# Kernel tuning notes

Measured on AMD Instinct MI355X. Metric: run time of the kernel, lower is better.

Reference implementation:

```python
import jax, jax.numpy as jnp
import numpy as np

N_ATOMS = 16384
B_GRAPHS = 64
K_CLUSTERS = 64          # clusters per molecule
M_CLUSTERS = B_GRAPHS * K_CLUSTERS
HID = 256                # hidden_channels (== node_attr feature dim)
FIL = 256                # num_filters
ECH = 64                 # edge_channels (num gaussians)
L_INT = 6                # num_interactions
CUTOFF = 10.0
LN2 = float(np.log(2.0))


def _ssp(x):
    # ShiftedSoftplus
    return jax.nn.softplus(x) - LN2


def setup_inputs() -> dict:
    key = jax.random.key(0)
    ks = jax.random.split(key, 12)
    pos = jax.random.normal(ks[0], (N_ATOMS, 3), jnp.float32) * 2.0
    node_attr = jax.random.normal(ks[1], (N_ATOMS, HID), jnp.float32)
    atoms_per_cluster = N_ATOMS // M_CLUSTERS
    subgraph_index = (jnp.arange(N_ATOMS) // atoms_per_cluster).astype(jnp.int64)
    batch = (jnp.arange(N_ATOMS) // (N_ATOMS // B_GRAPHS)).astype(jnp.int64)
    s = 0.05
    params = {
        "mlp_w1": jax.random.normal(ks[2], (L_INT, ECH, FIL), jnp.float32) * s,
        "mlp_b1": jnp.zeros((L_INT, FIL), jnp.float32),
        "mlp_w2": jax.random.normal(ks[3], (L_INT, FIL, FIL), jnp.float32) * s,
        "mlp_b2": jnp.zeros((L_INT, FIL), jnp.float32),
        "lin1_w": jax.random.normal(ks[4], (L_INT, HID, FIL), jnp.float32) * s,  # no bias
        "lin2_w": jax.random.normal(ks[5], (L_INT, FIL, HID), jnp.float32) * s,
        "lin2_b": jnp.zeros((L_INT, HID), jnp.float32),
        "lin_w":  jax.random.normal(ks[6], (L_INT, HID, HID), jnp.float32) * s,
        "lin_b":  jnp.zeros((L_INT, HID), jnp.float32),
    }
    return {"pos": pos, "node_attr": node_attr,
            "subgraph_index": subgraph_index, "batch": batch,
            "num_graphs": B_GRAPHS, "clusters_per_graph": K_CLUSTERS, **params}


def _complete_graph_edges(num_graphs, clusters_per_graph):
    # static (numpy) construction of per-molecule complete graph, no self loops
    K = clusters_per_graph
    i = np.arange(K)
    pr, pc = np.meshgrid(i, i, indexing='ij')
    m = pr != pc
    pr, pc = pr[m], pc[m]                       # (K*(K-1),)
    off = np.arange(num_graphs)[:, None] * K    # (B,1)
    row = jnp.asarray((off + pr[None, :]).reshape(-1))
    col = jnp.asarray((off + pc[None, :]).reshape(-1))
    return row, col


def reference(pos, node_attr, subgraph_index, batch, num_graphs, clusters_per_graph,
              mlp_w1, mlp_b1, mlp_w2, mlp_b2, lin1_w, lin2_w, lin2_b, lin_w, lin_b):
    M = num_graphs * clusters_per_graph
    # ---- coarse_grain: scatter-mean atoms into clusters ----
    cnt = jax.ops.segment_sum(jnp.ones((pos.shape[0],), pos.dtype), subgraph_index, num_segments=M)
    cnt = jnp.maximum(cnt, 1.0)[:, None]
    cluster_pos = jax.ops.segment_sum(pos, subgraph_index, num_segments=M) / cnt        # (M,3)
    cluster_attr = jax.ops.segment_sum(node_attr, subgraph_index, num_segments=M) / cnt  # (M,H)

    # ---- complete graph per molecule ----
    row, col = _complete_graph_edges(num_graphs, clusters_per_graph)
    edge_length = jnp.linalg.norm(cluster_pos[row] - cluster_pos[col], axis=1)          # (E,)

    # ---- GaussianSmearing ----
    offset = jnp.linspace(0.0, CUTOFF, ECH)
    coeff = -0.5 / (offset[1] - offset[0]) ** 2
    edge_attr = jnp.exp(coeff * (edge_length[:, None] - offset[None, :]) ** 2)          # (E,ECH)

    # smooth cutoff envelope
    C = 0.5 * (jnp.cos(edge_length * jnp.pi / CUTOFF) + 1.0)
    C = C * (edge_length <= CUTOFF).astype(C.dtype)                                     # (E,)

    # ---- SchNetEncoder (embed_node=False) ----
    h = cluster_attr
    for l in range(L_INT):
        # filter-generating MLP
        W = _ssp(edge_attr @ mlp_w1[l] + mlp_b1[l]) @ mlp_w2[l] + mlp_b2[l]             # (E,F)
        W = W * C[:, None]
        x = h @ lin1_w[l]                                                               # (M,F)
        agg = jax.ops.segment_sum(x[row] * W, col, num_segments=M)                      # (M,F)
        x = agg @ lin2_w[l] + lin2_b[l]                                                 # (M,H)
        x = _ssp(x)
        x = x @ lin_w[l] + lin_b[l]
        h = h + x                                                                       # residual
    return h
```

## Files before the change

kernel.cpp:

```cpp
#include <hip/hip_runtime.h>
#include <cstdint>

#define NATOMS 16384
#define BGRAPH 64
#define KC     64
#define MCL    (BGRAPH*KC)
#define HIDC   256
#define FILC   256
#define ECHC   64
#define LINT   6

#define TGRID  1024
#define TROWS  1088
#define NBP    1056

typedef __bf16 bf16x8 __attribute__((ext_vector_type(8)));
typedef __bf16 bf16x2 __attribute__((ext_vector_type(2)));
typedef float  f32x4  __attribute__((ext_vector_type(4)));
typedef unsigned short u16x8 __attribute__((ext_vector_type(8)));

__device__ __forceinline__ float bf2f(unsigned short u) {
    unsigned int x = ((unsigned int)u) << 16;
    return __builtin_bit_cast(float, x);
}
__device__ __forceinline__ unsigned short f2bf(float f) {
    __bf16 h = (__bf16)f;
    return __builtin_bit_cast(unsigned short, h);
}
__device__ __forceinline__ unsigned int pk2(float a, float b) {
    bf16x2 v = { (__bf16)a, (__bf16)b };
    return __builtin_bit_cast(unsigned int, v);
}
__device__ __forceinline__ float ssp_poly(float x) {
    float u = fminf(x * x, 4.0f);
    float q = u * fmaf(u, fmaf(u, 3.4722222e-4f, -5.2083333e-3f), 0.125f);
    return fmaf(0.5f, x, q);
}
__device__ __forceinline__ float ssp_fast(float x) {
    float m = fmaxf(x, 0.0f);
    float t = __builtin_amdgcn_exp2f(-fabsf(x) * 1.44269504088896341f);
    float l = __builtin_amdgcn_logf(1.0f + t);
    return fmaf(0.69314718055994531f, l, m - 0.69314718055994531f);
}
__device__ __forceinline__ int sw_off(int row, int col) {
    int s = (row + (row >> 3)) & 7;
    return row * 256 + ((((col >> 3) ^ s) << 3) | (col & 7));
}
__device__ __forceinline__ int phi_sw(int row) {
    return ((row & 7) ^ ((row >> 3) & 7)) & 7;
}

#define CGB   1024
#define N_W1  (LINT*16384)
#define N_BIG (LINT*65536)
#define PACK_BLOCKS ((N_W1 + 4*N_BIG + 255)/256)
__global__ void k_prep(const float* __restrict__ pos, const float* __restrict__ attr,
                       const int* __restrict__ subi,
                       float* __restrict__ h, unsigned short* __restrict__ h_bf,
                       float* __restrict__ cpos,
                       const float* __restrict__ w1_src, const float* __restrict__ w2_src,
                       const float* __restrict__ l1_src, const float* __restrict__ l2_src,
                       const float* __restrict__ lw_src,
                       unsigned short* __restrict__ w1p, unsigned short* __restrict__ w2p,
                       unsigned short* __restrict__ l1p, unsigned short* __restrict__ l2p,
                       unsigned short* __restrict__ lwp)
{
    if (blockIdx.x >= CGB) {
        int idx = (blockIdx.x - CGB) * 256 + threadIdx.x;
        if (idx < N_W1) {
            int j = idx & 7, lane = (idx >> 3) & 63, kt = (idx >> 9) & 1;
            int mt = (idx >> 10) & 15, l = idx >> 14;
            int ech = kt*32 + (lane >> 4)*8 + j;
            int f1  = mt*16 + (lane & 15);
            w1p[idx] = f2bf(w1_src[(l*64 + ech)*256 + f1]);
            return;
        }
        int r = idx - N_W1;
        int which = r / N_BIG;
        if (which >= 4) return;
        int e = r - which * N_BIG;
        const float* src = (which == 0) ? w2_src : (which == 1) ? l1_src
                         : (which == 2) ? l2_src : lw_src;
        unsigned short* dst = (which == 0) ? w2p : (which == 1) ? l1p
                            : (which == 2) ? l2p : lwp;
        int n = e % 256;
        int k = (e / 256) % 256;
        int l = e / 65536;
        int nt = n >> 4, kt = k >> 5, q = (k >> 3) & 3, j = k & 7;
        int lane = q*16 + (n & 15);
        dst[l*65536 + ((nt*8 + kt)*64 + lane)*8 + j] = f2bf(src[e]);
        return;
    }
    const int m = blockIdx.x * 4 + (threadIdx.x >> 6);
    const int lane = threadIdx.x & 63;
    const bool is64 = (subi[8] == 1);
    int lo = 0, hi = NATOMS;
    while (lo < hi) { int mid = (lo + hi) >> 1;
        int v = is64 ? subi[2*mid] : subi[mid];
        if (v < m) lo = mid + 1; else hi = mid; }
    int lo2 = lo, hi2 = NATOMS;
    while (lo2 < hi2) { int mid = (lo2 + hi2) >> 1;
        int v = is64 ? subi[2*mid] : subi[mid];
        if (v < m + 1) lo2 = mid + 1; else hi2 = mid; }
    const int cnt2 = lo2 - lo;
    const float inv = 1.0f / (float)(cnt2 > 0 ? cnt2 : 1);

    float4 s = {0.f, 0.f, 0.f, 0.f};
    for (int a = lo; a < lo2; a++) {
        const float4 v = *reinterpret_cast<const float4*>(&attr[a*HIDC + lane*4]);
        s.x += v.x; s.y += v.y; s.z += v.z; s.w += v.w;
    }
    s.x *= inv; s.y *= inv; s.z *= inv; s.w *= inv;
    *reinterpret_cast<float4*>(&h[m*HIDC + lane*4]) = s;
    const int o = m*HIDC + lane*4;
    h_bf[o+0] = f2bf(s.x); h_bf[o+1] = f2bf(s.y);
    h_bf[o+2] = f2bf(s.z); h_bf[o+3] = f2bf(s.w);
    if (lane < 3) {
        float p = 0.f;
        for (int a = lo; a < lo2; a++) p += pos[a*3 + lane];
        cpos[m*3 + lane] = p * inv;
    }
}

#define OSTR 264
__global__ __launch_bounds__(512, 6) void k_tab(
    const unsigned short* __restrict__ w1p_all, const unsigned short* __restrict__ w2p_all,
    const float* __restrict__ b1_all, const float* __restrict__ b2_all,
    unsigned short* __restrict__ table)
{
    __shared__ unsigned short G_s[64 * 256];
    __shared__ unsigned short phi_s[16 * OSTR];
    __shared__ float C_s[64];
    __shared__ float d_s[64];

    const int l  = blockIdx.x / 17;
    const int g0 = (blockIdx.x % 17) * 64;
    const unsigned short* w1p = w1p_all + (size_t)l*16384;
    const unsigned short* w2p = w2p_all + (size_t)l*65536;
    const float* b1 = b1_all + l*256;
    const float* b2 = b2_all + l*256;

    const int t  = threadIdx.x;
    const int w  = t >> 6, lane = t & 63;
    const int quad = lane >> 4, l16 = lane & 15;

    if (t < 64) {
        float d = (float)(g0 + t) * 0.009765625f;
        d_s[t] = d;
        float Cv = 0.5f * (__cosf(d * 0.31415926535897932f) + 1.0f);
        C_s[t] = (d <= 10.0f) ? Cv : 0.0f;
    }
    __syncthreads();

    const float DELTA = 10.0f / 63.0f;
    const float C2 = (-0.5f / (DELTA * DELTA)) * 1.44269504088896341f;
    {
        float d = d_s[lane];
        u16x8 ph;
        #pragma unroll
        for (int j = 0; j < 8; j++) {
            float diff = d - (float)(w*8 + j) * DELTA;
            ph[j] = f2bf(__builtin_amdgcn_exp2f(C2 * diff * diff));
        }
        *reinterpret_cast<u16x8*>(&phi_s[lane*64 + ((w ^ phi_sw(lane)) << 3)]) = ph;
    }
    __syncthreads();

    f32x4 acc1[2][4];
    #pragma unroll
    for (int mt = 0; mt < 2; mt++) {
        const int f1b = (w*2 + mt)*16 + quad*4;
        float4 bq = *reinterpret_cast<const float4*>(&b1[f1b]);
        #pragma unroll
        for (int nt = 0; nt < 4; nt++) {
            acc1[mt][nt][0] = bq.x; acc1[mt][nt][1] = bq.y;
            acc1[mt][nt][2] = bq.z; acc1[mt][nt][3] = bq.w;
        }
    }
    #pragma unroll
    for (int kt = 0; kt < 2; kt++) {
        bf16x8 bfr[4];
        #pragma unroll
        for (int nt = 0; nt < 4; nt++) {
            int row = nt*16 + l16;
            bfr[nt] = *reinterpret_cast<const bf16x8*>(
                &phi_s[row*64 + (((kt*4 + quad) ^ phi_sw(row)) << 3)]);
        }
        #pragma unroll
        for (int mt = 0; mt < 2; mt++) {
            bf16x8 afr = *reinterpret_cast<const bf16x8*>(
                w1p + (((w*2 + mt)*2 + kt)*64 + lane)*8);
            #pragma unroll
            for (int nt = 0; nt < 4; nt++)
                acc1[mt][nt] = __builtin_amdgcn_mfma_f32_16x16x32_bf16(afr, bfr[nt], acc1[mt][nt], 0, 0, 0);
        }
    }

    float Cn[4];
    #pragma unroll
    for (int nt = 0; nt < 4; nt++) Cn[nt] = C_s[nt*16 + l16];

    #pragma unroll
    for (int mt = 0; mt < 2; mt++) {
        const int f1b = (w*2 + mt)*16 + quad*4;
        #pragma unroll
        for (int nt = 0; nt < 4; nt++) {
            float v0 = ssp_poly(acc1[mt][nt][0]) * Cn[nt];
            float v1 = ssp_poly(acc1[mt][nt][1]) * Cn[nt];
            float v2 = ssp_poly(acc1[mt][nt][2]) * Cn[nt];
            float v3 = ssp_poly(acc1[mt][nt][3]) * Cn[nt];
            uint2 pp;
            pp.x = pk2(v0, v1);
            pp.y = pk2(v2, v3);
            int edge = nt*16 + l16;
            int s = (edge + (edge >> 3)) & 7;
            int a = edge*256 + ((((f1b >> 3) ^ s) << 3) | (f1b & 7));
            *reinterpret_cast<uint2*>(&G_s[a]) = pp;
        }
    }
    __syncthreads();

    f32x4 acc2[4][2];
    #pragma unroll
    for (int a = 0; a < 4; a++)
        #pragma unroll
        for (int bb = 0; bb < 2; bb++) acc2[a][bb] = f32x4{0.f,0.f,0.f,0.f};

    #pragma unroll
    for (int kt = 0; kt < 8; kt++) {
        bf16x8 afr[4];
        #pragma unroll
        for (int mt = 0; mt < 4; mt++) {
            int row = mt*16 + l16;
            int s = (row + (row >> 3)) & 7;
            afr[mt] = *reinterpret_cast<const bf16x8*>(&G_s[row*256 + (((kt*4 + quad) ^ s) << 3)]);
        }
        #pragma unroll
        for (int nt = 0; nt < 2; nt++) {
            const int ntg = w*2 + nt;
            bf16x8 bfr = *reinterpret_cast<const bf16x8*>(w2p + ((ntg*8 + kt)*64 + lane)*8);
            #pragma unroll
            for (int mt = 0; mt < 4; mt++)
                acc2[mt][nt] = __builtin_amdgcn_mfma_f32_16x16x32_bf16(afr[mt], bfr, acc2[mt][nt], 0, 0, 0);
        }
    }

    #pragma unroll
    for (int nt = 0; nt < 2; nt++) {
        const int f = (w*2 + nt)*16 + l16;
        const float b2v = b2[f];
        #pragma unroll
        for (int mt = 0; mt < 4; mt++) {
            #pragma unroll
            for (int i = 0; i < 4; i++) {
                int e = mt*16 + quad*4 + i;
                table[((size_t)l*TROWS + g0 + e)*256 + f] =
                    f2bf(fmaf(C_s[e], b2v, acc2[mt][nt][i]));
            }
        }
    }
}

__device__ __forceinline__ void gemm16(const unsigned short* A_s, const unsigned short* Bp,
                                       int w, int lane, f32x4 acc[4])
{
    const int quad = lane >> 4, l16 = lane & 15;
    const int s = (l16 + (l16 >> 3)) & 7;
    #pragma unroll
    for (int nt = 0; nt < 4; nt++) acc[nt] = f32x4{0.f,0.f,0.f,0.f};
    #pragma unroll
    for (int kt = 0; kt < 8; kt++) {
        bf16x8 afr = *reinterpret_cast<const bf16x8*>(&A_s[l16*256 + (((kt*4 + quad) ^ s) << 3)]);
        #pragma unroll
        for (int nt = 0; nt < 4; nt++) {
            bf16x8 bfr = *reinterpret_cast<const bf16x8*>(Bp + (((w*4 + nt)*8 + kt)*64 + lane)*8);
            acc[nt] = __builtin_amdgcn_mfma_f32_16x16x32_bf16(afr, bfr, acc[nt], 0, 0, 0);
        }
    }
}
__device__ __forceinline__ void gemm16w16(const unsigned short* A_s, const unsigned short* Bp,
                                          int w, int lane, f32x4& acc)
{
    const int quad = lane >> 4, l16 = lane & 15;
    const int s = (l16 + (l16 >> 3)) & 7;
    acc = f32x4{0.f,0.f,0.f,0.f};
    #pragma unroll
    for (int kt = 0; kt < 8; kt++) {
        bf16x8 afr = *reinterpret_cast<const bf16x8*>(&A_s[l16*256 + (((kt*4 + quad) ^ s) << 3)]);
        bf16x8 bfr = *reinterpret_cast<const bf16x8*>(Bp + (((w*8 + kt)*64 + lane))*8);
        acc = __builtin_amdgcn_mfma_f32_16x16x32_bf16(afr, bfr, acc, 0, 0, 0);
    }
}

#define PK_TOTAL (LINT*NBP*32)
#define PK_BLOCKS ((PK_TOTAL + 255)/256)
__global__ __launch_bounds__(256) void k_gemm0p(
    const unsigned short* __restrict__ A_bf, const unsigned short* __restrict__ Bp,
    unsigned short* __restrict__ out_bf,
    const unsigned short* __restrict__ table, unsigned short* __restrict__ tbl2)
{
    if (blockIdx.x >= 256) {
        int idx = (blockIdx.x - 256) * 256 + threadIdx.x;
        if (idx >= PK_TOTAL) return;
        int fc = idx & 31;
        int qq = idx >> 5;
        int bin = qq % NBP;
        int l = qq / NBP;
        if (bin > TGRID) return;
        const unsigned short* Ts = table + ((size_t)l*TROWS + bin)*256 + fc*8;
        u16x8 a = *reinterpret_cast<const u16x8*>(Ts);
        u16x8 b = *reinterpret_cast<const u16x8*>(Ts + 256);
        u16x8 d;
        #pragma unroll
        for (int j = 0; j < 8; j++) d[j] = f2bf(bf2f(b[j]) - bf2f(a[j]));
        unsigned short* dst = tbl2 + ((size_t)l*NBP + bin)*512 + fc*16;
        *reinterpret_cast<u16x8*>(dst)     = a;
        *reinterpret_cast<u16x8*>(dst + 8) = d;
        return;
    }
    __shared__ unsigned short A_s[16 * 256];
    const int mb = blockIdx.x;
    const int t = threadIdx.x;
    const int w = t >> 6, lane = t & 63, quad = lane >> 4, l16 = lane & 15;

    {
        int r = t >> 4, seg = t & 15;
        int s = (r + (r >> 3)) & 7;
        const u16x8* src = reinterpret_cast<const u16x8*>(A_bf + (size_t)(mb*16 + r)*256 + seg*16);
        int c = seg*2;
        *reinterpret_cast<u16x8*>(&A_s[r*256 + (((c  ) ^ s) << 3)]) = src[0];
        *reinterpret_cast<u16x8*>(&A_s[r*256 + (((c+1) ^ s) << 3)]) = src[1];
    }
    __syncthreads();

    f32x4 acc[4];
    gemm16(A_s, Bp, w, lane, acc);

    #pragma unroll
    for (int nt = 0; nt < 4; nt++)
        #pragma unroll
        for (int i = 0; i < 4; i++) {
            int rg = mb*16 + quad*4 + i;
            int col = w*64 + nt*16 + l16;
            out_bf[(size_t)rg*256 + col] = f2bf(acc[nt][i]);
        }
}

template<int DO_X>
__global__ __launch_bounds__(1024) void k_layer(
    const float* __restrict__ cpos,
    const unsigned short* __restrict__ xin, unsigned short* __restrict__ xout,
    const unsigned short* __restrict__ Tp,
    const unsigned short* __restrict__ lin2p, const float* __restrict__ lin2_b,
    const unsigned short* __restrict__ linp,  const float* __restrict__ lin_b,
    const unsigned short* __restrict__ lin1p,
    float* __restrict__ h)
{
    __shared__ unsigned short x_s[64 * 256];
    __shared__ unsigned short A0[16 * 256];
    __shared__ unsigned short A1[16 * 256];
    __shared__ int   idx_s[1024];
    __shared__ float frac_s[1024];

    const int blk = blockIdx.x;
    const int b = blk >> 2, q = blk & 3;
    const int t = threadIdx.x;
    const int w = t >> 6, lane = t & 63, quad = lane >> 4, l16 = lane & 15;

    {
        int r = t >> 4, seg = t & 15;
        const u16x8* s8 = reinterpret_cast<const u16x8*>(
            xin + ((size_t)(b*64 + r))*256 + seg*16);
        u16x8* dst = reinterpret_cast<u16x8*>(&x_s[r*256 + seg*16]);
        dst[0] = s8[0]; dst[1] = s8[1];
    }
    {
        int r = t >> 4, cc = t & 15;
        int gr = b*64 + r, gc = b*64 + q*16 + cc;
        float ax = cpos[gr*3 + 0] - cpos[gc*3 + 0];
        float ay = cpos[gr*3 + 1] - cpos[gc*3 + 1];
        float az = cpos[gr*3 + 2] - cpos[gc*3 + 2];
        float d = sqrtf(ax*ax + ay*ay + az*az);
        int i; float fr;
        if (gr == gc || d >= 10.0f) { i = TGRID; fr = 0.0f; }
        else {
            float u = d * 102.4f;
            i = (int)u; fr = u - (float)i;
        }
        idx_s[t] = i * 512; frac_s[t] = fr;
    }
    __syncthreads();

    const int fc  = t & 31;
    const int cp  = (t >> 5) & 7;
    const int dup = t >> 8;
    float s0[8] = {0.f,0.f,0.f,0.f,0.f,0.f,0.f,0.f};
    float s1[8] = {0.f,0.f,0.f,0.f,0.f,0.f,0.f,0.f};
    {
        const int rbase = dup * 16;
        const unsigned short* Tfc = Tp + fc*16;
        #pragma unroll 4
        for (int rr = 0; rr < 16; rr++) {
            const int r = rbase + rr;
            const int   p0 = idx_s [r*16 + cp];
            const float f0 = frac_s[r*16 + cp];
            const int   p1 = idx_s [r*16 + cp + 8];
            const float f1 = frac_s[r*16 + cp + 8];
            const u16x8 x8 = *reinterpret_cast<const u16x8*>(&x_s[r*256 + fc*8]);
            const u16x8 a0 = *reinterpret_cast<const u16x8*>(Tfc + p0);
            const u16x8 d0 = *reinterpret_cast<const u16x8*>(Tfc + p0 + 8);
            const u16x8 a1 = *reinterpret_cast<const u16x8*>(Tfc + p1);
            const u16x8 d1 = *reinterpret_cast<const u16x8*>(Tfc + p1 + 8);
            #pragma unroll
            for (int j = 0; j < 8; j++) {
                float xv = bf2f(x8[j]);
                float w0 = fmaf(f0, bf2f(d0[j]), bf2f(a0[j]));
                float w1 = fmaf(f1, bf2f(d1[j]), bf2f(a1[j]));
                s0[j] = fmaf(xv, w0, s0[j]);
                s1[j] = fmaf(xv, w1, s1[j]);
            }
        }
    }
    __syncthreads();
    {
        float* sc = reinterpret_cast<float*>(x_s);
        const int li = t & 255;
        if (dup & 1) {
            float* dst = sc + ((dup >> 1) << 12) + li*16;
            #pragma unroll
            for (int j = 0; j < 8; j++) { dst[j] = s0[j]; dst[8+j] = s1[j]; }
        }
        __syncthreads();
        if (!(dup & 1)) {
            const float* src = sc + ((dup >> 1) << 12) + li*16;
            #pragma unroll
            for (int j = 0; j < 8; j++) { s0[j] += src[j]; s1[j] += src[8+j]; }
        }
        __syncthreads();
        if (dup == 2) {
            float* dst = sc + li*16;
            #pragma unroll
            for (int j = 0; j < 8; j++) { dst[j] = s0[j]; dst[8+j] = s1[j]; }
        }
        __syncthreads();
        if (dup == 0) {
            const float* src = sc + li*16;
            u16x8 p0v, p1v;
            #pragma unroll
            for (int j = 0; j < 8; j++) {
                p0v[j] = f2bf(s0[j] + src[j]);
                p1v[j] = f2bf(s1[j] + src[8+j]);
            }
            const int c0 = cp, c1 = cp + 8;
            *reinterpret_cast<u16x8*>(&A0[c0*256 + ((fc ^ ((c0 + (c0>>3)) & 7)) << 3)]) = p0v;
            *reinterpret_cast<u16x8*>(&A0[c1*256 + ((fc ^ ((c1 + (c1>>3)) & 7)) << 3)]) = p1v;
        }
    }
    __syncthreads();

    const int col = w*16 + l16;
    const int rbase_g = b*64 + q*16;
    f32x4 acc;
    gemm16w16(A0, lin2p, w, lane, acc);
    float bv = lin2_b[col];
    #pragma unroll
    for (int i = 0; i < 4; i++)
        A1[sw_off(quad*4 + i, col)] = f2bf(ssp_fast(acc[i] + bv));
    __syncthreads();

    gemm16w16(A1, linp, w, lane, acc);
    bv = lin_b[col];
    float hv[4];
    #pragma unroll
    for (int i = 0; i < 4; i++) {
        int rg = rbase_g + quad*4 + i;
        float v = acc[i] + bv + h[(size_t)rg*256 + col];
        h[(size_t)rg*256 + col] = v;
        hv[i] = v;
    }
    if (DO_X) {
        #pragma unroll
        for (int i = 0; i < 4; i++)
            A0[sw_off(quad*4 + i, col)] = f2bf(hv[i]);
        __syncthreads();
        gemm16w16(A0, lin1p, w, lane, acc);
        #pragma unroll
        for (int i = 0; i < 4; i++) {
            int rg = rbase_g + quad*4 + i;
            xout[(size_t)rg*256 + col] = f2bf(acc[i]);
        }
    }
}

extern "C" void kernel_launch(void* const* d_in, const int* in_sizes, int n_in,
                              void* d_out, int out_size, void* d_ws, size_t ws_size,
                              hipStream_t stream)
{
    const float* pos    = (const float*)d_in[0];
    const float* nattr  = (const float*)d_in[1];
    const int*   subi   = (const int*)d_in[2];
    const float* mlp_w1 = (const float*)d_in[6];
    const float* mlp_b1 = (const float*)d_in[7];
    const float* mlp_w2 = (const float*)d_in[8];
    const float* mlp_b2 = (const float*)d_in[9];
    const float* lin1_w = (const float*)d_in[10];
    const float* lin2_w = (const float*)d_in[11];
    const float* lin2_b = (const float*)d_in[12];
    const float* lin_w  = (const float*)d_in[13];
    const float* lin_b  = (const float*)d_in[14];
    float* h = (float*)d_out;

    char* p = (char*)d_ws;
    auto alloc = [&](size_t bytes) { char* r = p; p += (bytes + 255) & ~(size_t)255; return r; };
    unsigned short* h_bf   = (unsigned short*)alloc((size_t)MCL*256*2);
    unsigned short* x0buf  = (unsigned short*)alloc((size_t)MCL*256*2);
    unsigned short* x1buf  = (unsigned short*)alloc((size_t)MCL*256*2);
    unsigned short* table  = (unsigned short*)alloc((size_t)LINT*TROWS*256*2);
    unsigned short* tbl2   = (unsigned short*)alloc((size_t)LINT*NBP*512*2);
    float*          cpos   = (float*)alloc((size_t)MCL*3*4);
    unsigned short* w1p    = (unsigned short*)alloc((size_t)LINT*16384*2);
    unsigned short* w2p    = (unsigned short*)alloc((size_t)LINT*65536*2);
    unsigned short* lin1p  = (unsigned short*)alloc((size_t)LINT*65536*2);
    unsigned short* lin2p  = (unsigned short*)alloc((size_t)LINT*65536*2);
    unsigned short* linp   = (unsigned short*)alloc((size_t)LINT*65536*2);

    k_prep<<<CGB + PACK_BLOCKS, 256, 0, stream>>>(
        pos, nattr, subi, h, h_bf, cpos,
        mlp_w1, mlp_w2, lin1_w, lin2_w, lin_w,
        w1p, w2p, lin1p, lin2p, linp);

    k_tab<<<LINT*17, 512, 0, stream>>>(w1p, w2p, mlp_b1, mlp_b2, table);

    k_gemm0p<<<256 + PK_BLOCKS, 256, 0, stream>>>(h_bf, lin1p, x0buf, table, tbl2);

    for (int l = 0; l < LINT; l++) {
        const unsigned short* xin  = (l & 1) ? x1buf : x0buf;
        unsigned short*       xout = (l & 1) ? x0buf : x1buf;
        const unsigned short* Tl = tbl2 + (size_t)l*NBP*512;
        if (l < LINT-1) {
            k_layer<1><<<BGRAPH*4, 1024, 0, stream>>>(cpos, xin, xout, Tl,
                lin2p + (size_t)l*65536, lin2_b + l*256,
                linp + (size_t)l*65536, lin_b + l*256,
                lin1p + (size_t)(l+1)*65536, h);
        } else {
            k_layer<0><<<BGRAPH*4, 1024, 0, stream>>>(cpos, xin, xout, Tl,
                lin2p + (size_t)l*65536, lin2_b + l*256,
                linp + (size_t)l*65536, lin_b + l*256,
                lin1p, h);
        }
    }
}
```

Measured before the change: 232.5 us.

## Remap edge aggregation so each wave owns one column with wave-uniform table rows

Changes the interleaved table layout from 8-wide to 4-wide value/delta groups and reworks the aggregation loop. Each wave now handles one destination cluster column, and each lane handles four filter channels across all 64 source rows. Because the table row index is the same across the wave, it is read with readfirstlane. This removes the cross-group shared-memory reduction and several barriers. In exchange each thread does more serial iterations with narrower per-thread vectors. The change assumes 1024 threads per block, i.e. 16 waves covering 16 columns.

After: 231.7 us. Within noise of the previous version (-0.4%).

```diff
diff --git a/kernel.cpp b/kernel.cpp
--- a/kernel.cpp
+++ b/kernel.cpp
@@ -292,7 +292,7 @@
     }
 }
 
-#define PK_TOTAL (LINT*NBP*32)
+#define PK_TOTAL (LINT*NBP*64)
 #define PK_BLOCKS ((PK_TOTAL + 255)/256)
 __global__ __launch_bounds__(256) void k_gemm0p(
     const unsigned short* __restrict__ A_bf, const unsigned short* __restrict__ Bp,
@@ -302,20 +302,22 @@
     if (blockIdx.x >= 256) {
         int idx = (blockIdx.x - 256) * 256 + threadIdx.x;
         if (idx >= PK_TOTAL) return;
-        int fc = idx & 31;
-        int qq = idx >> 5;
+        int fc2 = idx & 63;
+        int qq = idx >> 6;
         int bin = qq % NBP;
         int l = qq / NBP;
         if (bin > TGRID) return;
-        const unsigned short* Ts = table + ((size_t)l*TROWS + bin)*256 + fc*8;
-        u16x8 a = *reinterpret_cast<const u16x8*>(Ts);
-        u16x8 b = *reinterpret_cast<const u16x8*>(Ts + 256);
-        u16x8 d;
-        #pragma unroll
-        for (int j = 0; j < 8; j++) d[j] = f2bf(bf2f(b[j]) - bf2f(a[j]));
-        unsigned short* dst = tbl2 + ((size_t)l*NBP + bin)*512 + fc*16;
-        *reinterpret_cast<u16x8*>(dst)     = a;
-        *reinterpret_cast<u16x8*>(dst + 8) = d;
+        const unsigned short* Ts = table + ((size_t)l*TROWS + bin)*256 + fc2*4;
+        ushort4 a = *reinterpret_cast<const ushort4*>(Ts);
+        ushort4 b = *reinterpret_cast<const ushort4*>(Ts + 256);
+        ushort4 d;
+        d.x = f2bf(bf2f(b.x) - bf2f(a.x));
+        d.y = f2bf(bf2f(b.y) - bf2f(a.y));
+        d.z = f2bf(bf2f(b.z) - bf2f(a.z));
+        d.w = f2bf(bf2f(b.w) - bf2f(a.w));
+        unsigned short* dst = tbl2 + ((size_t)l*NBP + bin)*512 + fc2*8;
+        *reinterpret_cast<ushort4*>(dst)     = a;
+        *reinterpret_cast<ushort4*>(dst + 4) = d;
         return;
     }
     __shared__ unsigned short A_s[16 * 256];
@@ -391,70 +393,31 @@
     }
     __syncthreads();
 
-    const int fc  = t & 31;
-    const int cp  = (t >> 5) & 7;
-    const int dup = t >> 8;
-    float s0[8] = {0.f,0.f,0.f,0.f,0.f,0.f,0.f,0.f};
-    float s1[8] = {0.f,0.f,0.f,0.f,0.f,0.f,0.f,0.f};
     {
-        const int rbase = dup * 16;
-        const unsigned short* Tfc = Tp + fc*16;
-        #pragma unroll 4
-        for (int rr = 0; rr < 16; rr++) {
-            const int r = rbase + rr;
-            const int   p0 = idx_s [r*16 + cp];
-            const float f0 = frac_s[r*16 + cp];
-            const int   p1 = idx_s [r*16 + cp + 8];
-            const float f1 = frac_s[r*16 + cp + 8];
-            const u16x8 x8 = *reinterpret_cast<const u16x8*>(&x_s[r*256 + fc*8]);
-            const u16x8 a0 = *reinterpret_cast<const u16x8*>(Tfc + p0);
-            const u16x8 d0 = *reinterpret_cast<const u16x8*>(Tfc + p0 + 8);
-            const u16x8 a1 = *reinterpret_cast<const u16x8*>(Tfc + p1);
-            const u16x8 d1 = *reinterpret_cast<const u16x8*>(Tfc + p1 + 8);
-            #pragma unroll
-            for (int j = 0; j < 8; j++) {
-                float xv = bf2f(x8[j]);
-                float w0 = fmaf(f0, bf2f(d0[j]), bf2f(a0[j]));
-                float w1 = fmaf(f1, bf2f(d1[j]), bf2f(a1[j]));
-                s0[j] = fmaf(xv, w0, s0[j]);
-                s1[j] = fmaf(xv, w1, s1[j]);
-            }
-        }
-    }
-    __syncthreads();
-    {
-        float* sc = reinterpret_cast<float*>(x_s);
-        const int li = t & 255;
-        if (dup & 1) {
-            float* dst = sc + ((dup >> 1) << 12) + li*16;
-            #pragma unroll
-            for (int j = 0; j < 8; j++) { dst[j] = s0[j]; dst[8+j] = s1[j]; }
-        }
-        __syncthreads();
-        if (!(dup & 1)) {
-            const float* src = sc + ((dup >> 1) << 12) + li*16;
-            #pragma unroll
-            for (int j = 0; j < 8; j++) { s0[j] += src[j]; s1[j] += src[8+j]; }
-        }
-        __syncthreads();
-        if (dup == 2) {
-            float* dst = sc + li*16;
-            #pragma unroll
-            for (int j = 0; j < 8; j++) { dst[j] = s0[j]; dst[8+j] = s1[j]; }
-        }
-        __syncthreads();
-        if (dup == 0) {
-            const float* src = sc + li*16;
-            u16x8 p0v, p1v;
-            #pragma unroll
-            for (int j = 0; j < 8; j++) {
-                p0v[j] = f2bf(s0[j] + src[j]);
-                p1v[j] = f2bf(s1[j] + src[8+j]);
-            }
-            const int c0 = cp, c1 = cp + 8;
-            *reinterpret_cast<u16x8*>(&A0[c0*256 + ((fc ^ ((c0 + (c0>>3)) & 7)) << 3)]) = p0v;
-            *reinterpret_cast<u16x8*>(&A0[c1*256 + ((fc ^ ((c1 + (c1>>3)) & 7)) << 3)]) = p1v;
-        }
+        const int c   = t >> 6;
+        const int fc2 = t & 63;
+        float a4[4] = {0.f, 0.f, 0.f, 0.f};
+        #pragma unroll 8
+        for (int r = 0; r < 64; r++) {
+            const int   pi = __builtin_amdgcn_readfirstlane(idx_s[r*16 + c]);
+            const float fr = frac_s[r*16 + c];
+            const u16x8 td = *reinterpret_cast<const u16x8*>(Tp + pi + fc2*8);
+            const ushort4 x4 = *reinterpret_cast<const ushort4*>(&x_s[r*256 + fc2*4]);
+            float w0 = fmaf(fr, bf2f(td[4]), bf2f(td[0]));
+            float w1 = fmaf(fr, bf2f(td[5]), bf2f(td[1]));
+            float w2 = fmaf(fr, bf2f(td[6]), bf2f(td[2]));
+            float w3 = fmaf(fr, bf2f(td[7]), bf2f(td[3]));
+            a4[0] = fmaf(bf2f(x4.x), w0, a4[0]);
+            a4[1] = fmaf(bf2f(x4.y), w1, a4[1]);
+            a4[2] = fmaf(bf2f(x4.z), w2, a4[2]);
+            a4[3] = fmaf(bf2f(x4.w), w3, a4[3]);
+        }
+        uint2 pv;
+        pv.x = pk2(a4[0], a4[1]);
+        pv.y = pk2(a4[2], a4[3]);
+        int s2 = (c + (c >> 3)) & 7;
+        *reinterpret_cast<uint2*>(
+            &A0[c*256 + ((((fc2 >> 1) ^ s2) << 3) | ((fc2 & 1) * 4))]) = pv;
     }
     __syncthreads();
 
```
